# Kernel tuning notes

Measured on AMD Instinct MI355X. Metric: run time of the kernel, lower is better.

## Reference

```python
import jax, jax.numpy as jnp
import numpy as np

N, R, IN_DIM, OUT_DIM, MODE = 8, 256, 64, 64, 32


def setup_inputs() -> dict:
    key = jax.random.key(0)
    k_x, k_w0, k_w1, k_rw, k_rb = jax.random.split(key, 5)
    scale = (1.0 / (IN_DIM * OUT_DIM)) * np.sqrt(IN_DIM + OUT_DIM)
    return {
        "x": jax.random.normal(k_x, (N, R, R, IN_DIM), dtype=jnp.float32),
        # real/imag stacked, matching torch Parameter [m, m, in, out, 2]
        "w0": jax.random.normal(k_w0, (MODE, MODE, IN_DIM, OUT_DIM, 2), dtype=jnp.float32) * scale,
        "w1": jax.random.normal(k_w1, (MODE, MODE, IN_DIM, OUT_DIM, 2), dtype=jnp.float32) * scale,
        # residual Linear: stored as [in, out] (torch keeps [out, in]; math identical)
        "res_w": jax.random.normal(k_rw, (IN_DIM, OUT_DIM), dtype=jnp.float32) * 0.05,
        "res_b": jax.random.normal(k_rb, (OUT_DIM,), dtype=jnp.float32) * 0.05,
    }


def reference(x, w0, w1, res_w, res_b):
    n, r, _, in_dim = x.shape
    m = w0.shape[0]
    rc = r // 2 + 1
    out_dim = w0.shape[3]

    # residual branch (Linear)
    res = jnp.einsum("nhwi,io->nhwo", x, res_w) + res_b  # [N, r, r, out]

    # channels-first for 2D FFT over spatial dims (droprate = 0 -> no dropout)
    xt = jnp.transpose(x, (0, 3, 1, 2))                    # [N, in, r, r]
    x_ft = jnp.fft.rfft2(xt, s=(r, r), norm="ortho")       # [N, in, r, rc] complex

    # gather low-frequency mode blocks: rows [0:m] and [r-m:r], cols [0:m]
    blk0 = x_ft[:, :, :m, :m]                              # [N, in, m, m]
    blk1 = x_ft[:, :, r - m:, :m]                          # [N, in, m, m]

    W0 = w0[..., 0] + 1j * w0[..., 1]                      # [m, m, in, out]
    W1 = w1[..., 0] + 1j * w1[..., 1]

    out0 = jnp.einsum("nixy,xyio->noxy", blk0, W0)         # [N, out, m, m]
    out1 = jnp.einsum("nixy,xyio->noxy", blk1, W1)

    # scatter back into zero-initialized full spectrum
    out_ft = jnp.zeros((n, out_dim, r, rc), dtype=out0.dtype)
    out_ft = out_ft.at[:, :, :m, :m].set(out0)
    out_ft = out_ft.at[:, :, r - m:, :m].set(out1)

    y = jnp.fft.irfft2(out_ft, s=(r, r), norm="ortho")     # [N, out, r, r]
    y = jnp.transpose(y, (0, 2, 3, 1))                     # [N, r, r, out]
    return jax.nn.silu(y + res)
```

## Files before the change

### kernel.cpp

```cpp
#include <hip/hip_runtime.h>
#include <math.h>

#define NN 8
#define RR 256
#define CD 64
#define MM 32
#define KHN 64
#define KWN 32

#define ANG 0.024543692606170259f
#define INVN (1.0f / 65536.0f)

typedef __attribute__((ext_vector_type(4))) float f32x4;
typedef __attribute__((ext_vector_type(8))) short short8;
typedef unsigned short u16;

__device__ inline u16 f2bf(float f) {
    union { float f; unsigned u; } v; v.f = f;
    unsigned r = v.u + 0x7FFF + ((v.u >> 16) & 1);
    return (u16)(r >> 16);
}
__device__ inline unsigned pack2(float a, float b) {
    return (unsigned)f2bf(a) | ((unsigned)f2bf(b) << 16);
}
__device__ inline int swkey(int row) { return (row & 7) ^ ((row >> 3) & 7); }

__global__ __launch_bounds__(256) void k0_tables(u16* __restrict__ A2g,
                                                 u16* __restrict__ A4g,
                                                 u16* __restrict__ T1g,
                                                 u16* __restrict__ T5g,
                                                 const float* __restrict__ res_w,
                                                 u16* __restrict__ RWTg) {
    int gid = blockIdx.x * 256 + threadIdx.x;
    {
        int r = gid >> 9, k = gid & 511;
        int khIdx = r & 63, part = r >> 6;
        int kh = (khIdx < 32) ? khIdx : 192 + khIdx;
        int h = k & 255, kpart = k >> 8;
        float s, c;
        __sincosf((float)((kh * h) & 255) * ANG, &s, &c);
        float v = (part == 0) ? ((kpart == 0) ? c : s)
                              : ((kpart == 0) ? -s : c);
        A2g[gid] = f2bf(v);
    }
    {
        int r = gid >> 7, k = gid & 127;
        int h = r & 255, part = r >> 8;
        int khIdx = k & 63, kpart = k >> 6;
        int kh = (khIdx < 32) ? khIdx : 192 + khIdx;
        float s, c;
        __sincosf((float)((kh * h) & 255) * ANG, &s, &c);
        float v = (part == 0) ? ((kpart == 0) ? c : -s)
                              : ((kpart == 0) ? s : c);
        A4g[gid] = f2bf(v);
    }
    if (gid < 16384) {
        {
            int r = gid >> 8, w = gid & 255;
            float s, c;
            if (r < 32) { __sincosf((float)((r * w) & 255) * ANG, &s, &c); T1g[gid] = f2bf(c); }
            else        { __sincosf((float)(((r - 32) * w) & 255) * ANG, &s, &c); T1g[gid] = f2bf(-s); }
        }
        {
            int w = gid >> 6, c = gid & 63;
            float v;
            if (c == 0) v = 1.0f;
            else if (c < 32) { float s, co; __sincosf((float)((c * w) & 255) * ANG, &s, &co); v = 2.0f * co; }
            else if (c == 32) v = 0.0f;
            else { float s, co; __sincosf((float)(((c - 32) * w) & 255) * ANG, &s, &co); v = -2.0f * s; }
            T5g[gid] = f2bf(v);
        }
    }
    if (gid < 4096) {
        int o = gid >> 6, i = gid & 63;
        RWTg[gid] = f2bf(res_w[i * 64 + o]);
    }
}

__global__ __launch_bounds__(256) void k1_dft_w(const float* __restrict__ x,
                                                const u16* __restrict__ T1g,
                                                u16* __restrict__ X1R,
                                                u16* __restrict__ X1I) {
    __shared__ __align__(16) u16 Bt[64 * 256];
    unsigned* B32 = (unsigned*)Bt;
    int t = threadIdx.x;
    int nh = blockIdx.x;
    const float* xr = x + (size_t)nh * (RR * CD);
#pragma unroll
    for (int it = 0; it < 8; ++it) {
        int idx = t + it * 256;
        int q = idx >> 4;
        int c0 = (idx & 15) * 4;
        float4 f0 = *(const float4*)&xr[(2 * q) * 64 + c0];
        float4 f1 = *(const float4*)&xr[(2 * q + 1) * 64 + c0];
        B32[(c0 + 0) * 128 + (q ^ (swkey(c0 + 0) << 2))] = pack2(f0.x, f1.x);
        B32[(c0 + 1) * 128 + (q ^ (swkey(c0 + 1) << 2))] = pack2(f0.y, f1.y);
        B32[(c0 + 2) * 128 + (q ^ (swkey(c0 + 2) << 2))] = pack2(f0.z, f1.z);
        B32[(c0 + 3) * 128 + (q ^ (swkey(c0 + 3) << 2))] = pack2(f0.w, f1.w);
    }
    __syncthreads();
    int wv = t >> 6, l = t & 63, lm = l & 15, lq = l >> 4;
    f32x4 acc[4];
#pragma unroll
    for (int nt = 0; nt < 4; ++nt) { f32x4 z = {0.f, 0.f, 0.f, 0.f}; acc[nt] = z; }
#pragma unroll
    for (int ks = 0; ks < 8; ++ks) {
        short8 a = *(const short8*)&T1g[(wv * 16 + lm) * 256 + ks * 32 + lq * 8];
#pragma unroll
        for (int nt = 0; nt < 4; ++nt) {
            int c = nt * 16 + lm;
            short8 b = *(const short8*)&Bt[c * 256 + ((ks * 32 + lq * 8) ^ (swkey(c) << 3))];
            acc[nt] = __builtin_amdgcn_mfma_f32_16x16x32_bf16(a, b, acc[nt], 0, 0, 0);
        }
    }
    int n = nh >> 8, h = nh & 255;
#pragma unroll
    for (int nt = 0; nt < 4; ++nt)
#pragma unroll
        for (int r = 0; r < 4; ++r) {
            int kwp = wv * 16 + lq * 4 + r;
            int cc = nt * 16 + lm;
            u16 v = f2bf(acc[nt][r]);
            if (kwp < 32) X1R[(((size_t)n * 32 + kwp) * 256 + h) * 64 + cc] = v;
            else          X1I[(((size_t)n * 32 + (kwp - 32)) * 256 + h) * 64 + cc] = v;
        }
}

__global__ __launch_bounds__(512) void k2_dft_h(const u16* __restrict__ X1R,
                                                const u16* __restrict__ X1I,
                                                const u16* __restrict__ A2g,
                                                float2* __restrict__ X2) {
    __shared__ __align__(16) u16 Bs[2][64 * 128];
    int t = threadIdx.x;
    int n = blockIdx.x >> 5, kw = blockIdx.x & 31;
    const u16* baseR = X1R + ((size_t)n * 32 + kw) * (256 * 64);
    const u16* baseI = X1I + ((size_t)n * 32 + kw) * (256 * 64);
    int wv = t >> 6, l = t & 63, lm = l & 15, lq = l >> 4;
    f32x4 acc[4];
#pragma unroll
    for (int nt = 0; nt < 4; ++nt) { f32x4 z = {0.f, 0.f, 0.f, 0.f}; acc[nt] = z; }

    auto stage = [&](int ck, int buf) {
        const u16* src = ((ck < 2) ? baseR : baseI) + (size_t)(ck & 1) * (128 * 64);
        u16* B = Bs[buf];
#pragma unroll
        for (int it = 0; it < 2; ++it) {
            int idx = t + it * 512;
            int hh = idx >> 3, g = idx & 7;
            short8 v = *(const short8*)&src[hh * 64 + g * 8];
#pragma unroll
            for (int j = 0; j < 8; ++j) {
                int c = g * 8 + j;
                B[c * 128 + (hh ^ (swkey(c) << 3))] = (u16)v[j];
            }
        }
    };
    stage(0, 0);
    __syncthreads();
    for (int ck = 0; ck < 4; ++ck) {
        if (ck < 3) stage(ck + 1, (ck + 1) & 1);
        const u16* B = Bs[ck & 1];
#pragma unroll
        for (int ks = 0; ks < 4; ++ks) {
            short8 a = *(const short8*)&A2g[(wv * 16 + lm) * 512 + ck * 128 + ks * 32 + lq * 8];
#pragma unroll
            for (int nt = 0; nt < 4; ++nt) {
                int c = nt * 16 + lm;
                short8 b = *(const short8*)&B[c * 128 + ((ks * 32 + lq * 8) ^ (swkey(c) << 3))];
                acc[nt] = __builtin_amdgcn_mfma_f32_16x16x32_bf16(a, b, acc[nt], 0, 0, 0);
            }
        }
        __syncthreads();
    }
#pragma unroll
    for (int nt = 0; nt < 4; ++nt)
#pragma unroll
        for (int r = 0; r < 4; ++r) {
            int m = wv * 16 + lq * 4 + r;
            int c = nt * 16 + lm;
            float* dst = (float*)&X2[(((size_t)n * 64 + (m & 63)) * 32 + kw) * 64 + c];
            dst[m >> 6] = acc[nt][r];
        }
}

__global__ __launch_bounds__(256) void k3_spectral(const float2* __restrict__ X2,
                                                   const float* __restrict__ w0,
                                                   const float* __restrict__ w1,
                                                   unsigned* __restrict__ X3b) {
    __shared__ float2 WsP[4096];
    __shared__ float2 XsP[512];
    int t = threadIdx.x;
    int khIdx = blockIdx.x >> 5;
    int kw = blockIdx.x & 31;
    const float* wsrc = (khIdx < 32)
        ? (w0 + (size_t)(khIdx * 32 + kw) * (64 * 64 * 2))
        : (w1 + (size_t)((khIdx - 32) * 32 + kw) * (64 * 64 * 2));
    const float4* wsrc4 = (const float4*)wsrc;
#pragma unroll
    for (int k = 0; k < 8; ++k) {
        int idx = t + k * 256;
        float4 v = wsrc4[idx];
        WsP[2 * idx]     = make_float2(v.x * INVN, v.y * INVN);
        WsP[2 * idx + 1] = make_float2(v.z * INVN, v.w * INVN);
    }
#pragma unroll
    for (int k = 0; k < 2; ++k) {
        int id2 = t + k * 256;
        int n = id2 >> 6, c = id2 & 63;
        XsP[id2] = X2[(((size_t)n * KHN + khIdx) * KWN + kw) * CD + c];
    }
    __syncthreads();
    int o = t & 63;
    int ng = t >> 6;
#pragma unroll
    for (int p = 0; p < 2; ++p) {
        int n = ng + p * 4;
        float aR = 0.f, aI = 0.f;
#pragma unroll 8
        for (int i = 0; i < 64; ++i) {
            float2 xv = XsP[n * 64 + i];
            float2 wv_ = WsP[i * 64 + o];
            aR += xv.x * wv_.x - xv.y * wv_.y;
            aI += xv.x * wv_.y + xv.y * wv_.x;
        }
        X3b[(((size_t)n * 32 + kw) * 64 + khIdx) * 64 + o] = pack2(aR, aI);
    }
}

__global__ __launch_bounds__(256) void k4_idft_h(const unsigned* __restrict__ X3b,
                                                 const u16* __restrict__ A4g,
                                                 u16* __restrict__ Y1R,
                                                 u16* __restrict__ Y1I) {
    __shared__ __align__(16) u16 Bs[64 * 128];
    int t = threadIdx.x;
    int b = blockIdx.x;
    int n = b >> 7, kw = (b >> 2) & 31, mh = (b >> 1) & 1, ac = b & 1;
    const unsigned* src = X3b + ((size_t)n * 32 + kw) * (64 * 64);
#pragma unroll
    for (int it = 0; it < 16; ++it) {
        int khl = (t & 7) + ((it & 7) << 3);
        int o = ((t >> 3) & 31) + ((it >> 3) << 5);
        unsigned v = src[khl * 64 + o];
        int K = swkey(o) << 3;
        Bs[o * 128 + (khl ^ K)]        = (u16)(v & 0xFFFF);
        Bs[o * 128 + ((64 + khl) ^ K)] = (u16)(v >> 16);
    }
    __syncthreads();
    int wv = t >> 6, l = t & 63, lm = l & 15, lq = l >> 4;
    u16* plane = mh ? Y1I : Y1R;
    f32x4 acc[2][4];
#pragma unroll
    for (int mt = 0; mt < 2; ++mt)
#pragma unroll
        for (int nt = 0; nt < 4; ++nt) { f32x4 z = {0.f, 0.f, 0.f, 0.f}; acc[mt][nt] = z; }
#pragma unroll
    for (int ks = 0; ks < 4; ++ks) {
        short8 a0 = *(const short8*)&A4g[(size_t)(mh * 256 + ac * 128 + wv * 32 + lm) * 128 + ks * 32 + lq * 8];
        short8 a1 = *(const short8*)&A4g[(size_t)(mh * 256 + ac * 128 + wv * 32 + 16 + lm) * 128 + ks * 32 + lq * 8];
#pragma unroll
        for (int nt = 0; nt < 4; ++nt) {
            int c = nt * 16 + lm;
            short8 bfr = *(const short8*)&Bs[c * 128 + ((ks * 32 + lq * 8) ^ (swkey(c) << 3))];
            acc[0][nt] = __builtin_amdgcn_mfma_f32_16x16x32_bf16(a0, bfr, acc[0][nt], 0, 0, 0);
            acc[1][nt] = __builtin_amdgcn_mfma_f32_16x16x32_bf16(a1, bfr, acc[1][nt], 0, 0, 0);
        }
    }
#pragma unroll
    for (int mt = 0; mt < 2; ++mt)
#pragma unroll
        for (int nt = 0; nt < 4; ++nt)
#pragma unroll
            for (int r = 0; r < 4; ++r) {
                int h = ac * 128 + wv * 32 + mt * 16 + lq * 4 + r;
                int o = nt * 16 + lm;
                plane[(((size_t)n * 256 + h) * 32 + kw) * 64 + o] = f2bf(acc[mt][nt][r]);
            }
}

__global__ __launch_bounds__(256) void k5_final(const u16* __restrict__ YRp,
                                                const u16* __restrict__ YIp,
                                                const float* __restrict__ x,
                                                const float* __restrict__ res_b,
                                                const u16* __restrict__ T5g,
                                                const u16* __restrict__ RWTg,
                                                float* __restrict__ out) {
    __shared__ __align__(16) u16 Xs[128 * 64];
    __shared__ __align__(16) u16 Bs[64 * 128];
    __shared__ float bs[64];
    unsigned* X32 = (unsigned*)Xs;
    unsigned* B32 = (unsigned*)Bs;
    int t = threadIdx.x;
    int nh = blockIdx.x >> 1, half = blockIdx.x & 1;
    if (t < 64) bs[t] = res_b[t];
    const float* xb = x + ((size_t)nh * 256 + half * 128) * 64;
#pragma unroll
    for (int it = 0; it < 8; ++it) {
        int idx = t + it * 256;
        int wl = idx >> 4, c4 = idx & 15;
        float4 f = *(const float4*)&xb[wl * 64 + c4 * 4];
        uint2 pv; pv.x = pack2(f.x, f.y); pv.y = pack2(f.z, f.w);
        *(uint2*)&X32[wl * 32 + ((2 * c4) ^ (swkey(wl) << 2))] = pv;
    }
    const u16* YR = YRp + (size_t)nh * 2048;
    const u16* YI = YIp + (size_t)nh * 2048;
#pragma unroll
    for (int it = 0; it < 8; ++it) {
        int kw = t >> 3;
        int op = (t & 7) + (it & 3) * 8;
        const u16* P = (it >> 2) ? YI : YR;
        unsigned v = *(const unsigned*)&P[kw * 64 + 2 * op];
        int k = (it >> 2) * 32 + kw;
        int o0 = 2 * op;
        Bs[o0 * 128 + (k ^ (swkey(o0) << 3))]       = (u16)(v & 0xFFFF);
        Bs[(o0 + 1) * 128 + (k ^ (swkey(o0 + 1) << 3))] = (u16)(v >> 16);
    }
#pragma unroll
    for (int it = 0; it < 2; ++it) {
        int idx = t + it * 256;
        int o = idx >> 3, g = idx & 7;
        uint4 v = *(const uint4*)&RWTg[o * 64 + g * 8];
        *(uint4*)&B32[o * 64 + (8 + (g ^ swkey(o))) * 4] = v;
    }
    __syncthreads();
    int wv = t >> 6, l = t & 63, lm = l & 15, lq = l >> 4;
    f32x4 acc[2][4];
#pragma unroll
    for (int mt = 0; mt < 2; ++mt)
#pragma unroll
        for (int nt = 0; nt < 4; ++nt) { f32x4 z = {0.f, 0.f, 0.f, 0.f}; acc[mt][nt] = z; }
#pragma unroll
    for (int ks = 0; ks < 4; ++ks) {
        int r0 = wv * 32 + lm, r1 = r0 + 16;
        short8 a0, a1;
        if (ks < 2) {
            a0 = *(const short8*)&T5g[(half * 128 + r0) * 64 + ks * 32 + lq * 8];
            a1 = *(const short8*)&T5g[(half * 128 + r1) * 64 + ks * 32 + lq * 8];
        } else {
            a0 = *(const short8*)&Xs[r0 * 64 + (((ks - 2) * 32 + lq * 8) ^ (swkey(r0) << 3))];
            a1 = *(const short8*)&Xs[r1 * 64 + (((ks - 2) * 32 + lq * 8) ^ (swkey(r1) << 3))];
        }
#pragma unroll
        for (int nt = 0; nt < 4; ++nt) {
            int c = nt * 16 + lm;
            short8 b = *(const short8*)&Bs[c * 128 + ((ks * 32 + lq * 8) ^ (swkey(c) << 3))];
            acc[0][nt] = __builtin_amdgcn_mfma_f32_16x16x32_bf16(a0, b, acc[0][nt], 0, 0, 0);
            acc[1][nt] = __builtin_amdgcn_mfma_f32_16x16x32_bf16(a1, b, acc[1][nt], 0, 0, 0);
        }
    }
    float* orow = out + ((size_t)nh * 256 + half * 128) * 64;
#pragma unroll
    for (int mt = 0; mt < 2; ++mt)
#pragma unroll
        for (int nt = 0; nt < 4; ++nt)
#pragma unroll
            for (int r = 0; r < 4; ++r) {
                int wloc = wv * 32 + mt * 16 + lq * 4 + r;
                int o = nt * 16 + lm;
                float v = acc[mt][nt][r] + bs[o];
                float sv = v / (1.0f + __expf(-v));
                orow[wloc * 64 + o] = sv;
            }
}

extern "C" void kernel_launch(void* const* d_in, const int* in_sizes, int n_in,
                              void* d_out, int out_size, void* d_ws, size_t ws_size,
                              hipStream_t stream) {
    const float* x     = (const float*)d_in[0];
    const float* w0    = (const float*)d_in[1];
    const float* w1    = (const float*)d_in[2];
    const float* res_w = (const float*)d_in[3];
    const float* res_b = (const float*)d_in[4];
    float* out = (float*)d_out;
    char* ws = (char*)d_ws;
    u16*      X1R  = (u16*)(ws);
    u16*      X1I  = (u16*)(ws + 8388608);
    float2*   X2   = (float2*)(ws + 16777216);
    unsigned* X3b  = (unsigned*)(ws + 25165824);
    u16*      Y1R  = (u16*)(ws + 33554432);
    u16*      Y1I  = (u16*)(ws + 41943040);
    u16*      A2g  = (u16*)(ws + 50331648);
    u16*      A4g  = (u16*)(ws + 50462720);
    u16*      T1g  = (u16*)(ws + 50593792);
    u16*      T5g  = (u16*)(ws + 50626560);
    u16*      RWTg = (u16*)(ws + 50659328);

    k0_tables  <<<256,          256, 0, stream>>>(A2g, A4g, T1g, T5g, res_w, RWTg);
    k1_dft_w   <<<NN * RR,      256, 0, stream>>>(x, T1g, X1R, X1I);
    k2_dft_h   <<<NN * KWN,     512, 0, stream>>>(X1R, X1I, A2g, X2);
    k3_spectral<<<KHN * KWN,    256, 0, stream>>>(X2, w0, w1, X3b);
    k4_idft_h  <<<NN * KWN * 4, 256, 0, stream>>>(X3b, A4g, Y1R, Y1I);
    k5_final   <<<NN * RR * 2,  256, 0, stream>>>(Y1R, Y1I, x, res_b, T5g, RWTg, out);
}
```

Baseline: 352.6 us.

## Fuse six FFT-stage kernels into one cooperative persistent kernel with grid syncs

```diff
diff --git a/kernel.cpp b/kernel.cpp
--- a/kernel.cpp
+++ b/kernel.cpp
@@ -1,5 +1,8 @@
 #include <hip/hip_runtime.h>
+#include <hip/hip_cooperative_groups.h>
 #include <math.h>
+
+namespace cg = cooperative_groups;
 
 #define NN 8
 #define RR 256
@@ -24,6 +27,369 @@
     return (unsigned)f2bf(a) | ((unsigned)f2bf(b) << 16);
 }
 __device__ inline int swkey(int row) { return (row & 7) ^ ((row >> 3) & 7); }
+
+__global__ __launch_bounds__(256, 4) void mega(
+    const float* __restrict__ x, const float* __restrict__ w0,
+    const float* __restrict__ w1, const float* __restrict__ res_w,
+    const float* __restrict__ res_b,
+    u16* __restrict__ X1R, u16* __restrict__ X1I,
+    float2* __restrict__ X2, unsigned* __restrict__ X3b,
+    u16* __restrict__ Y1R, u16* __restrict__ Y1I,
+    u16* __restrict__ A2g, u16* __restrict__ A4g,
+    u16* __restrict__ T1g, u16* __restrict__ T5g,
+    u16* __restrict__ RWTg, float* __restrict__ out)
+{
+    cg::grid_group grid = cg::this_grid();
+    __shared__ __align__(16) unsigned char SMEM[37120];
+    int t = threadIdx.x;
+    int b = blockIdx.x;
+    int G = gridDim.x;
+    int wv = t >> 6, l = t & 63, lm = l & 15, lq = l >> 4;
+
+    {
+        int gid = b * 256 + t;
+        if (gid < 65536) {
+            {
+                int r = gid >> 9, k = gid & 511;
+                int khIdx = r & 63, part = r >> 6;
+                int kh = (khIdx < 32) ? khIdx : 192 + khIdx;
+                int h = k & 255, kpart = k >> 8;
+                float s, c;
+                __sincosf((float)((kh * h) & 255) * ANG, &s, &c);
+                float v = (part == 0) ? ((kpart == 0) ? c : s)
+                                      : ((kpart == 0) ? -s : c);
+                A2g[gid] = f2bf(v);
+            }
+            {
+                int r = gid >> 7, k = gid & 127;
+                int h = r & 255, part = r >> 8;
+                int khIdx = k & 63, kpart = k >> 6;
+                int kh = (khIdx < 32) ? khIdx : 192 + khIdx;
+                float s, c;
+                __sincosf((float)((kh * h) & 255) * ANG, &s, &c);
+                float v = (part == 0) ? ((kpart == 0) ? c : -s)
+                                      : ((kpart == 0) ? s : c);
+                A4g[gid] = f2bf(v);
+            }
+            if (gid < 16384) {
+                {
+                    int r = gid >> 8, w = gid & 255;
+                    float s, c;
+                    if (r < 32) { __sincosf((float)((r * w) & 255) * ANG, &s, &c); T1g[gid] = f2bf(c); }
+                    else        { __sincosf((float)(((r - 32) * w) & 255) * ANG, &s, &c); T1g[gid] = f2bf(-s); }
+                }
+                {
+                    int w = gid >> 6, c = gid & 63;
+                    float v;
+                    if (c == 0) v = 1.0f;
+                    else if (c < 32) { float s, co; __sincosf((float)((c * w) & 255) * ANG, &s, &co); v = 2.0f * co; }
+                    else if (c == 32) v = 0.0f;
+                    else { float s, co; __sincosf((float)(((c - 32) * w) & 255) * ANG, &s, &co); v = -2.0f * s; }
+                    T5g[gid] = f2bf(v);
+                }
+            }
+            if (gid < 4096) {
+                int o = gid >> 6, i = gid & 63;
+                RWTg[gid] = f2bf(res_w[i * 64 + o]);
+            }
+        }
+    }
+    __threadfence();
+    grid.sync();
+
+    {
+        u16* Bt = (u16*)SMEM;
+        unsigned* B32 = (unsigned*)SMEM;
+        for (int nh = b; nh < NN * RR; nh += G) {
+            const float* xr = x + (size_t)nh * (RR * CD);
+#pragma unroll
+            for (int it = 0; it < 8; ++it) {
+                int idx = t + it * 256;
+                int q = idx >> 4;
+                int c0 = (idx & 15) * 4;
+                float4 f0 = *(const float4*)&xr[(2 * q) * 64 + c0];
+                float4 f1 = *(const float4*)&xr[(2 * q + 1) * 64 + c0];
+                B32[(c0 + 0) * 128 + (q ^ (swkey(c0 + 0) << 2))] = pack2(f0.x, f1.x);
+                B32[(c0 + 1) * 128 + (q ^ (swkey(c0 + 1) << 2))] = pack2(f0.y, f1.y);
+                B32[(c0 + 2) * 128 + (q ^ (swkey(c0 + 2) << 2))] = pack2(f0.z, f1.z);
+                B32[(c0 + 3) * 128 + (q ^ (swkey(c0 + 3) << 2))] = pack2(f0.w, f1.w);
+            }
+            __syncthreads();
+            f32x4 acc[4];
+#pragma unroll
+            for (int nt = 0; nt < 4; ++nt) { f32x4 z = {0.f, 0.f, 0.f, 0.f}; acc[nt] = z; }
+#pragma unroll
+            for (int ks = 0; ks < 8; ++ks) {
+                short8 a = *(const short8*)&T1g[(wv * 16 + lm) * 256 + ks * 32 + lq * 8];
+#pragma unroll
+                for (int nt = 0; nt < 4; ++nt) {
+                    int c = nt * 16 + lm;
+                    short8 bf = *(const short8*)&Bt[c * 256 + ((ks * 32 + lq * 8) ^ (swkey(c) << 3))];
+                    acc[nt] = __builtin_amdgcn_mfma_f32_16x16x32_bf16(a, bf, acc[nt], 0, 0, 0);
+                }
+            }
+            int n = nh >> 8, h = nh & 255;
+#pragma unroll
+            for (int nt = 0; nt < 4; ++nt)
+#pragma unroll
+                for (int r = 0; r < 4; ++r) {
+                    int kwp = wv * 16 + lq * 4 + r;
+                    int cc = nt * 16 + lm;
+                    u16 v = f2bf(acc[nt][r]);
+                    if (kwp < 32) X1R[(((size_t)n * 32 + kwp) * 256 + h) * 64 + cc] = v;
+                    else          X1I[(((size_t)n * 32 + (kwp - 32)) * 256 + h) * 64 + cc] = v;
+                }
+            __syncthreads();
+        }
+    }
+    __threadfence();
+    grid.sync();
+
+    {
+        u16* Bs0 = (u16*)SMEM;
+        u16* Bs1 = (u16*)(SMEM + 16384);
+        for (int tile = b; tile < NN * KWN; tile += G) {
+            int n = tile >> 5, kw = tile & 31;
+            const u16* baseR = X1R + ((size_t)n * 32 + kw) * (256 * 64);
+            const u16* baseI = X1I + ((size_t)n * 32 + kw) * (256 * 64);
+            f32x4 acc[2][4];
+#pragma unroll
+            for (int mt = 0; mt < 2; ++mt)
+#pragma unroll
+                for (int nt = 0; nt < 4; ++nt) { f32x4 z = {0.f, 0.f, 0.f, 0.f}; acc[mt][nt] = z; }
+            auto stage = [&](int ck, u16* Bp) {
+                const u16* src = ((ck < 2) ? baseR : baseI) + (size_t)(ck & 1) * (128 * 64);
+                unsigned* B32 = (unsigned*)Bp;
+#pragma unroll
+                for (int it = 0; it < 2; ++it) {
+                    int idx = t + it * 256;
+                    int hh2 = idx >> 3;
+                    int g = idx & 7;
+                    short8 v0 = *(const short8*)&src[(2 * hh2) * 64 + g * 8];
+                    short8 v1 = *(const short8*)&src[(2 * hh2 + 1) * 64 + g * 8];
+#pragma unroll
+                    for (int j = 0; j < 8; ++j) {
+                        int c = g * 8 + j;
+                        B32[c * 64 + (hh2 ^ (swkey(c) << 2))] =
+                            (unsigned)(u16)v0[j] | ((unsigned)(u16)v1[j] << 16);
+                    }
+                }
+            };
+            stage(0, Bs0);
+            __syncthreads();
+            for (int ck = 0; ck < 4; ++ck) {
+                if (ck < 3) stage(ck + 1, ((ck + 1) & 1) ? Bs1 : Bs0);
+                const u16* B = (ck & 1) ? Bs1 : Bs0;
+#pragma unroll
+                for (int ks = 0; ks < 4; ++ks) {
+                    short8 a0 = *(const short8*)&A2g[(wv * 32 + lm) * 512 + ck * 128 + ks * 32 + lq * 8];
+                    short8 a1 = *(const short8*)&A2g[(wv * 32 + 16 + lm) * 512 + ck * 128 + ks * 32 + lq * 8];
+#pragma unroll
+                    for (int nt = 0; nt < 4; ++nt) {
+                        int c = nt * 16 + lm;
+                        short8 bf = *(const short8*)&B[c * 128 + ((ks * 32 + lq * 8) ^ (swkey(c) << 3))];
+                        acc[0][nt] = __builtin_amdgcn_mfma_f32_16x16x32_bf16(a0, bf, acc[0][nt], 0, 0, 0);
+                        acc[1][nt] = __builtin_amdgcn_mfma_f32_16x16x32_bf16(a1, bf, acc[1][nt], 0, 0, 0);
+                    }
+                }
+                __syncthreads();
+            }
+#pragma unroll
+            for (int mt = 0; mt < 2; ++mt)
+#pragma unroll
+                for (int nt = 0; nt < 4; ++nt)
+#pragma unroll
+                    for (int r = 0; r < 4; ++r) {
+                        int m = wv * 32 + mt * 16 + lq * 4 + r;
+                        int c = nt * 16 + lm;
+                        float* dst = (float*)&X2[(((size_t)n * 64 + (m & 63)) * 32 + kw) * 64 + c];
+                        dst[m >> 6] = acc[mt][nt][r];
+                    }
+            __syncthreads();
+        }
+    }
+    __threadfence();
+    grid.sync();
+
+    {
+        float2* WsP = (float2*)SMEM;
+        float2* XsP = (float2*)(SMEM + 32768);
+        for (int tile = b; tile < KHN * KWN; tile += G) {
+            int khIdx = tile >> 5;
+            int kw = tile & 31;
+            const float* wsrc = (khIdx < 32)
+                ? (w0 + (size_t)(khIdx * 32 + kw) * (64 * 64 * 2))
+                : (w1 + (size_t)((khIdx - 32) * 32 + kw) * (64 * 64 * 2));
+            const float4* wsrc4 = (const float4*)wsrc;
+#pragma unroll
+            for (int k = 0; k < 8; ++k) {
+                int idx = t + k * 256;
+                float4 v = wsrc4[idx];
+                WsP[2 * idx]     = make_float2(v.x * INVN, v.y * INVN);
+                WsP[2 * idx + 1] = make_float2(v.z * INVN, v.w * INVN);
+            }
+#pragma unroll
+            for (int k = 0; k < 2; ++k) {
+                int id2 = t + k * 256;
+                int n = id2 >> 6, c = id2 & 63;
+                XsP[id2] = X2[(((size_t)n * KHN + khIdx) * KWN + kw) * CD + c];
+            }
+            __syncthreads();
+            int o = t & 63;
+            int ng = t >> 6;
+#pragma unroll
+            for (int p = 0; p < 2; ++p) {
+                int n = ng + p * 4;
+                float aR = 0.f, aI = 0.f;
+#pragma unroll 8
+                for (int i = 0; i < 64; ++i) {
+                    float2 xv = XsP[n * 64 + i];
+                    float2 wv_ = WsP[i * 64 + o];
+                    aR += xv.x * wv_.x - xv.y * wv_.y;
+                    aI += xv.x * wv_.y + xv.y * wv_.x;
+                }
+                X3b[(((size_t)n * 32 + kw) * 64 + khIdx) * 64 + o] = pack2(aR, aI);
+            }
+            __syncthreads();
+        }
+    }
+    __threadfence();
+    grid.sync();
+
+    {
+        u16* Bs = (u16*)SMEM;
+        unsigned* B32 = (unsigned*)SMEM;
+        for (int tile = b; tile < NN * KWN * 4; tile += G) {
+            int n = tile >> 7, kw = (tile >> 2) & 31, mh = (tile >> 1) & 1, ac = tile & 1;
+            const unsigned* src = X3b + ((size_t)n * 32 + kw) * (64 * 64);
+#pragma unroll
+            for (int it = 0; it < 8; ++it) {
+                int idx = t + it * 256;
+                int khl2 = idx >> 6;
+                int o = idx & 63;
+                unsigned vA = src[(2 * khl2) * 64 + o];
+                unsigned vB = src[(2 * khl2 + 1) * 64 + o];
+                int K = swkey(o) << 2;
+                B32[o * 64 + (khl2 ^ K)]        = (vA & 0xFFFF) | (vB << 16);
+                B32[o * 64 + ((32 + khl2) ^ K)] = (vA >> 16) | (vB & 0xFFFF0000u);
+            }
+            __syncthreads();
+            u16* plane = mh ? Y1I : Y1R;
+            f32x4 acc[2][4];
+#pragma unroll
+            for (int mt = 0; mt < 2; ++mt)
+#pragma unroll
+                for (int nt = 0; nt < 4; ++nt) { f32x4 z = {0.f, 0.f, 0.f, 0.f}; acc[mt][nt] = z; }
+#pragma unroll
+            for (int ks = 0; ks < 4; ++ks) {
+                short8 a0 = *(const short8*)&A4g[(size_t)(mh * 256 + ac * 128 + wv * 32 + lm) * 128 + ks * 32 + lq * 8];
+                short8 a1 = *(const short8*)&A4g[(size_t)(mh * 256 + ac * 128 + wv * 32 + 16 + lm) * 128 + ks * 32 + lq * 8];
+#pragma unroll
+                for (int nt = 0; nt < 4; ++nt) {
+                    int c = nt * 16 + lm;
+                    short8 bfr = *(const short8*)&Bs[c * 128 + ((ks * 32 + lq * 8) ^ (swkey(c) << 3))];
+                    acc[0][nt] = __builtin_amdgcn_mfma_f32_16x16x32_bf16(a0, bfr, acc[0][nt], 0, 0, 0);
+                    acc[1][nt] = __builtin_amdgcn_mfma_f32_16x16x32_bf16(a1, bfr, acc[1][nt], 0, 0, 0);
+                }
+            }
+#pragma unroll
+            for (int mt = 0; mt < 2; ++mt)
+#pragma unroll
+                for (int nt = 0; nt < 4; ++nt)
+#pragma unroll
+                    for (int r = 0; r < 4; ++r) {
+                        int h = ac * 128 + wv * 32 + mt * 16 + lq * 4 + r;
+                        int o = nt * 16 + lm;
+                        plane[(((size_t)n * 256 + h) * 32 + kw) * 64 + o] = f2bf(acc[mt][nt][r]);
+                    }
+            __syncthreads();
+        }
+    }
+    __threadfence();
+    grid.sync();
+
+    {
+        u16* Xs = (u16*)SMEM;
+        u16* Bs = (u16*)(SMEM + 16384);
+        float* bsm = (float*)(SMEM + 32768);
+        unsigned* X32 = (unsigned*)Xs;
+        unsigned* B32 = (unsigned*)Bs;
+        if (t < 64) bsm[t] = res_b[t];
+        for (int bb = b; bb < NN * RR * 2; bb += G) {
+            int nh = bb >> 1, half = bb & 1;
+            const float* xb = x + ((size_t)nh * 256 + half * 128) * 64;
+#pragma unroll
+            for (int it = 0; it < 8; ++it) {
+                int idx = t + it * 256;
+                int wl = idx >> 4, c4 = idx & 15;
+                float4 f = *(const float4*)&xb[wl * 64 + c4 * 4];
+                uint2 pv; pv.x = pack2(f.x, f.y); pv.y = pack2(f.z, f.w);
+                *(uint2*)&X32[wl * 32 + ((2 * c4) ^ (swkey(wl) << 2))] = pv;
+            }
+            const u16* YR = Y1R + (size_t)nh * 2048;
+            const u16* YI = Y1I + (size_t)nh * 2048;
+#pragma unroll
+            for (int it = 0; it < 4; ++it) {
+                int part = it >> 1;
+                int kw2 = t >> 4;
+                int opb = (t & 15) + (it & 1) * 16;
+                const u16* P = part ? YI : YR;
+                unsigned vA = *(const unsigned*)&P[(2 * kw2) * 64 + 2 * opb];
+                unsigned vB = *(const unsigned*)&P[(2 * kw2 + 1) * 64 + 2 * opb];
+                int o0 = 2 * opb;
+                int k2 = part * 16 + kw2;
+                B32[o0 * 64 + (k2 ^ (swkey(o0) << 2))]       = (vA & 0xFFFF) | (vB << 16);
+                B32[(o0 + 1) * 64 + (k2 ^ (swkey(o0 + 1) << 2))] = (vA >> 16) | (vB & 0xFFFF0000u);
+            }
+#pragma unroll
+            for (int it = 0; it < 2; ++it) {
+                int idx = t + it * 256;
+                int o = idx >> 3, g = idx & 7;
+                uint4 v = *(const uint4*)&RWTg[o * 64 + g * 8];
+                *(uint4*)&B32[o * 64 + (8 + (g ^ swkey(o))) * 4] = v;
+            }
+            __syncthreads();
+            f32x4 acc[2][4];
+#pragma unroll
+            for (int mt = 0; mt < 2; ++mt)
+#pragma unroll
+                for (int nt = 0; nt < 4; ++nt) { f32x4 z = {0.f, 0.f, 0.f, 0.f}; acc[mt][nt] = z; }
+#pragma unroll
+            for (int ks = 0; ks < 4; ++ks) {
+                int r0 = wv * 32 + lm, r1 = r0 + 16;
+                short8 a0, a1;
+                if (ks < 2) {
+                    a0 = *(const short8*)&T5g[(half * 128 + r0) * 64 + ks * 32 + lq * 8];
+                    a1 = *(const short8*)&T5g[(half * 128 + r1) * 64 + ks * 32 + lq * 8];
+                } else {
+                    a0 = *(const short8*)&Xs[r0 * 64 + (((ks - 2) * 32 + lq * 8) ^ (swkey(r0) << 3))];
+                    a1 = *(const short8*)&Xs[r1 * 64 + (((ks - 2) * 32 + lq * 8) ^ (swkey(r1) << 3))];
+                }
+#pragma unroll
+                for (int nt = 0; nt < 4; ++nt) {
+                    int c = nt * 16 + lm;
+                    short8 bf = *(const short8*)&Bs[c * 128 + ((ks * 32 + lq * 8) ^ (swkey(c) << 3))];
+                    acc[0][nt] = __builtin_amdgcn_mfma_f32_16x16x32_bf16(a0, bf, acc[0][nt], 0, 0, 0);
+                    acc[1][nt] = __builtin_amdgcn_mfma_f32_16x16x32_bf16(a1, bf, acc[1][nt], 0, 0, 0);
+                }
+            }
+            float* orow = out + ((size_t)nh * 256 + half * 128) * 64;
+#pragma unroll
+            for (int mt = 0; mt < 2; ++mt)
+#pragma unroll
+                for (int nt = 0; nt < 4; ++nt)
+#pragma unroll
+                    for (int r = 0; r < 4; ++r) {
+                        int wloc = wv * 32 + mt * 16 + lq * 4 + r;
+                        int o = nt * 16 + lm;
+                        float v = acc[mt][nt][r] + bsm[o];
+                        float sv = v / (1.0f + __expf(-v));
+                        orow[wloc * 64 + o] = sv;
+                    }
+            __syncthreads();
+        }
+    }
+}
 
 __global__ __launch_bounds__(256) void k0_tables(u16* __restrict__ A2g,
                                                  u16* __restrict__ A4g,
@@ -39,8 +405,7 @@
         int h = k & 255, kpart = k >> 8;
         float s, c;
         __sincosf((float)((kh * h) & 255) * ANG, &s, &c);
-        float v = (part == 0) ? ((kpart == 0) ? c : s)
-                              : ((kpart == 0) ? -s : c);
+        float v = (part == 0) ? ((kpart == 0) ? c : s) : ((kpart == 0) ? -s : c);
         A2g[gid] = f2bf(v);
     }
     {
@@ -50,8 +415,7 @@
         int kh = (khIdx < 32) ? khIdx : 192 + khIdx;
         float s, c;
         __sincosf((float)((kh * h) & 255) * ANG, &s, &c);
-        float v = (part == 0) ? ((kpart == 0) ? c : -s)
-                              : ((kpart == 0) ? s : c);
+        float v = (part == 0) ? ((kpart == 0) ? c : -s) : ((kpart == 0) ? s : c);
         A4g[gid] = f2bf(v);
     }
     if (gid < 16384) {
@@ -109,8 +473,8 @@
 #pragma unroll
         for (int nt = 0; nt < 4; ++nt) {
             int c = nt * 16 + lm;
-            short8 b = *(const short8*)&Bt[c * 256 + ((ks * 32 + lq * 8) ^ (swkey(c) << 3))];
-            acc[nt] = __builtin_amdgcn_mfma_f32_16x16x32_bf16(a, b, acc[nt], 0, 0, 0);
+            short8 bf = *(const short8*)&Bt[c * 256 + ((ks * 32 + lq * 8) ^ (swkey(c) << 3))];
+            acc[nt] = __builtin_amdgcn_mfma_f32_16x16x32_bf16(a, bf, acc[nt], 0, 0, 0);
         }
     }
     int n = nh >> 8, h = nh & 255;
@@ -139,7 +503,6 @@
     f32x4 acc[4];
 #pragma unroll
     for (int nt = 0; nt < 4; ++nt) { f32x4 z = {0.f, 0.f, 0.f, 0.f}; acc[nt] = z; }
-
     auto stage = [&](int ck, int buf) {
         const u16* src = ((ck < 2) ? baseR : baseI) + (size_t)(ck & 1) * (128 * 64);
         u16* B = Bs[buf];
@@ -166,8 +529,8 @@
 #pragma unroll
             for (int nt = 0; nt < 4; ++nt) {
                 int c = nt * 16 + lm;
-                short8 b = *(const short8*)&B[c * 128 + ((ks * 32 + lq * 8) ^ (swkey(c) << 3))];
-                acc[nt] = __builtin_amdgcn_mfma_f32_16x16x32_bf16(a, b, acc[nt], 0, 0, 0);
+                short8 bf = *(const short8*)&B[c * 128 + ((ks * 32 + lq * 8) ^ (swkey(c) << 3))];
+                acc[nt] = __builtin_amdgcn_mfma_f32_16x16x32_bf16(a, bf, acc[nt], 0, 0, 0);
             }
         }
         __syncthreads();
@@ -232,18 +595,21 @@
                                                  u16* __restrict__ Y1R,
                                                  u16* __restrict__ Y1I) {
     __shared__ __align__(16) u16 Bs[64 * 128];
+    unsigned* B32 = (unsigned*)Bs;
     int t = threadIdx.x;
     int b = blockIdx.x;
     int n = b >> 7, kw = (b >> 2) & 31, mh = (b >> 1) & 1, ac = b & 1;
     const unsigned* src = X3b + ((size_t)n * 32 + kw) * (64 * 64);
 #pragma unroll
-    for (int it = 0; it < 16; ++it) {
-        int khl = (t & 7) + ((it & 7) << 3);
-        int o = ((t >> 3) & 31) + ((it >> 3) << 5);
-        unsigned v = src[khl * 64 + o];
-        int K = swkey(o) << 3;
-        Bs[o * 128 + (khl ^ K)]        = (u16)(v & 0xFFFF);
-        Bs[o * 128 + ((64 + khl) ^ K)] = (u16)(v >> 16);
+    for (int it = 0; it < 8; ++it) {
+        int idx = t + it * 256;
+        int khl2 = idx >> 6;
+        int o = idx & 63;
+        unsigned vA = src[(2 * khl2) * 64 + o];
+        unsigned vB = src[(2 * khl2 + 1) * 64 + o];
+        int K = swkey(o) << 2;
+        B32[o * 64 + (khl2 ^ K)]        = (vA & 0xFFFF) | (vB << 16);
+        B32[o * 64 + ((32 + khl2) ^ K)] = (vA >> 16) | (vB & 0xFFFF0000u);
     }
     __syncthreads();
     int wv = t >> 6, l = t & 63, lm = l & 15, lq = l >> 4;
@@ -304,15 +670,17 @@
     const u16* YR = YRp + (size_t)nh * 2048;
     const u16* YI = YIp + (size_t)nh * 2048;
 #pragma unroll
-    for (int it = 0; it < 8; ++it) {
-        int kw = t >> 3;
-        int op = (t & 7) + (it & 3) * 8;
-        const u16* P = (it >> 2) ? YI : YR;
-        unsigned v = *(const unsigned*)&P[kw * 64 + 2 * op];
-        int k = (it >> 2) * 32 + kw;
-        int o0 = 2 * op;
-        Bs[o0 * 128 + (k ^ (swkey(o0) << 3))]       = (u16)(v & 0xFFFF);
-        Bs[(o0 + 1) * 128 + (k ^ (swkey(o0 + 1) << 3))] = (u16)(v >> 16);
+    for (int it = 0; it < 4; ++it) {
+        int part = it >> 1;
+        int kw2 = t >> 4;
+        int opb = (t & 15) + (it & 1) * 16;
+        const u16* P = part ? YI : YR;
+        unsigned vA = *(const unsigned*)&P[(2 * kw2) * 64 + 2 * opb];
+        unsigned vB = *(const unsigned*)&P[(2 * kw2 + 1) * 64 + 2 * opb];
+        int o0 = 2 * opb;
+        int k2 = part * 16 + kw2;
+        B32[o0 * 64 + (k2 ^ (swkey(o0) << 2))]       = (vA & 0xFFFF) | (vB << 16);
+        B32[(o0 + 1) * 64 + (k2 ^ (swkey(o0 + 1) << 2))] = (vA >> 16) | (vB & 0xFFFF0000u);
     }
 #pragma unroll
     for (int it = 0; it < 2; ++it) {
@@ -342,9 +710,9 @@
 #pragma unroll
         for (int nt = 0; nt < 4; ++nt) {
             int c = nt * 16 + lm;
-            short8 b = *(const short8*)&Bs[c * 128 + ((ks * 32 + lq * 8) ^ (swkey(c) << 3))];
-            acc[0][nt] = __builtin_amdgcn_mfma_f32_16x16x32_bf16(a0, b, acc[0][nt], 0, 0, 0);
-            acc[1][nt] = __builtin_amdgcn_mfma_f32_16x16x32_bf16(a1, b, acc[1][nt], 0, 0, 0);
+            short8 bf = *(const short8*)&Bs[c * 128 + ((ks * 32 + lq * 8) ^ (swkey(c) << 3))];
+            acc[0][nt] = __builtin_amdgcn_mfma_f32_16x16x32_bf16(a0, bf, acc[0][nt], 0, 0, 0);
+            acc[1][nt] = __builtin_amdgcn_mfma_f32_16x16x32_bf16(a1, bf, acc[1][nt], 0, 0, 0);
         }
     }
     float* orow = out + ((size_t)nh * 256 + half * 128) * 64;
@@ -384,10 +752,27 @@
     u16*      T5g  = (u16*)(ws + 50626560);
     u16*      RWTg = (u16*)(ws + 50659328);
 
-    k0_tables  <<<256,          256, 0, stream>>>(A2g, A4g, T1g, T5g, res_w, RWTg);
-    k1_dft_w   <<<NN * RR,      256, 0, stream>>>(x, T1g, X1R, X1I);
-    k2_dft_h   <<<NN * KWN,     512, 0, stream>>>(X1R, X1I, A2g, X2);
-    k3_spectral<<<KHN * KWN,    256, 0, stream>>>(X2, w0, w1, X3b);
-    k4_idft_h  <<<NN * KWN * 4, 256, 0, stream>>>(X3b, A4g, Y1R, Y1I);
-    k5_final   <<<NN * RR * 2,  256, 0, stream>>>(Y1R, Y1I, x, res_b, T5g, RWTg, out);
-}
+    static int G = 0;
+    if (G == 0) {
+        int nb = 0;
+        if (hipOccupancyMaxActiveBlocksPerMultiprocessor(&nb, mega, 256, 0) != hipSuccess || nb < 1)
+            nb = 1;
+        if (nb > 4) nb = 4;
+        G = nb * 256;
+    }
+
+    void* args[] = { (void*)&x, (void*)&w0, (void*)&w1, (void*)&res_w, (void*)&res_b,
+                     (void*)&X1R, (void*)&X1I, (void*)&X2, (void*)&X3b,
+                     (void*)&Y1R, (void*)&Y1I, (void*)&A2g, (void*)&A4g,
+                     (void*)&T1g, (void*)&T5g, (void*)&RWTg, (void*)&out };
+    hipError_t e = hipLaunchCooperativeKernel((const void*)mega, dim3(G), dim3(256),
+                                              args, 0, stream);
+    if (e != hipSuccess) {
+        k0_tables  <<<256,          256, 0, stream>>>(A2g, A4g, T1g, T5g, res_w, RWTg);
+        k1_dft_w   <<<NN * RR,      256, 0, stream>>>(x, T1g, X1R, X1I);
+        k2_dft_h   <<<NN * KWN,     512, 0, stream>>>(X1R, X1I, A2g, X2);
+        k3_spectral<<<KHN * KWN,    256, 0, stream>>>(X2, w0, w1, X3b);
+        k4_idft_h  <<<NN * KWN * 4, 256, 0, stream>>>(X3b, A4g, Y1R, Y1I);
+        k5_final   <<<NN * RR * 2,  256, 0, stream>>>(Y1R, Y1I, x, res_b, T5g, RWTg, out);
+    }
+}
```

Result: slower. 895.4 us (+153.9%).

## Fuse forward H-DFT, spectral mixing and inverse H-DFT into one kernel

Applied to the files above, without the earlier changes.

```diff
diff --git a/kernel.cpp b/kernel.cpp
--- a/kernel.cpp
+++ b/kernel.cpp
@@ -39,8 +39,7 @@
         int h = k & 255, kpart = k >> 8;
         float s, c;
         __sincosf((float)((kh * h) & 255) * ANG, &s, &c);
-        float v = (part == 0) ? ((kpart == 0) ? c : s)
-                              : ((kpart == 0) ? -s : c);
+        float v = (part == 0) ? ((kpart == 0) ? c : s) : ((kpart == 0) ? -s : c);
         A2g[gid] = f2bf(v);
     }
     {
@@ -50,8 +49,7 @@
         int kh = (khIdx < 32) ? khIdx : 192 + khIdx;
         float s, c;
         __sincosf((float)((kh * h) & 255) * ANG, &s, &c);
-        float v = (part == 0) ? ((kpart == 0) ? c : -s)
-                              : ((kpart == 0) ? s : c);
+        float v = (part == 0) ? ((kpart == 0) ? c : -s) : ((kpart == 0) ? s : c);
         A4g[gid] = f2bf(v);
     }
     if (gid < 16384) {
@@ -109,8 +107,8 @@
 #pragma unroll
         for (int nt = 0; nt < 4; ++nt) {
             int c = nt * 16 + lm;
-            short8 b = *(const short8*)&Bt[c * 256 + ((ks * 32 + lq * 8) ^ (swkey(c) << 3))];
-            acc[nt] = __builtin_amdgcn_mfma_f32_16x16x32_bf16(a, b, acc[nt], 0, 0, 0);
+            short8 bf = *(const short8*)&Bt[c * 256 + ((ks * 32 + lq * 8) ^ (swkey(c) << 3))];
+            acc[nt] = __builtin_amdgcn_mfma_f32_16x16x32_bf16(a, bf, acc[nt], 0, 0, 0);
         }
     }
     int n = nh >> 8, h = nh & 255;
@@ -126,23 +124,30 @@
         }
 }
 
-__global__ __launch_bounds__(512) void k2_dft_h(const u16* __restrict__ X1R,
-                                                const u16* __restrict__ X1I,
-                                                const u16* __restrict__ A2g,
-                                                float2* __restrict__ X2) {
-    __shared__ __align__(16) u16 Bs[2][64 * 128];
+__global__ __launch_bounds__(512) void k234(const u16* __restrict__ X1R,
+                                            const u16* __restrict__ X1I,
+                                            const u16* __restrict__ A2g,
+                                            const float* __restrict__ w0,
+                                            const float* __restrict__ w1,
+                                            const u16* __restrict__ A4g,
+                                            u16* __restrict__ Y1R,
+                                            u16* __restrict__ Y1I) {
+    __shared__ __align__(16) unsigned char SMEM[49664];
+    u16* Bs0 = (u16*)SMEM;
+    u16* Bs1 = (u16*)(SMEM + 16384);
+    float* Xsp = (float*)SMEM;
+    u16* X3s = (u16*)(SMEM + 33280);
     int t = threadIdx.x;
     int n = blockIdx.x >> 5, kw = blockIdx.x & 31;
     const u16* baseR = X1R + ((size_t)n * 32 + kw) * (256 * 64);
     const u16* baseI = X1I + ((size_t)n * 32 + kw) * (256 * 64);
     int wv = t >> 6, l = t & 63, lm = l & 15, lq = l >> 4;
+
     f32x4 acc[4];
 #pragma unroll
     for (int nt = 0; nt < 4; ++nt) { f32x4 z = {0.f, 0.f, 0.f, 0.f}; acc[nt] = z; }
-
-    auto stage = [&](int ck, int buf) {
+    auto stage = [&](int ck, u16* B) {
         const u16* src = ((ck < 2) ? baseR : baseI) + (size_t)(ck & 1) * (128 * 64);
-        u16* B = Bs[buf];
 #pragma unroll
         for (int it = 0; it < 2; ++it) {
             int idx = t + it * 512;
@@ -155,19 +160,19 @@
             }
         }
     };
-    stage(0, 0);
+    stage(0, Bs0);
     __syncthreads();
     for (int ck = 0; ck < 4; ++ck) {
-        if (ck < 3) stage(ck + 1, (ck + 1) & 1);
-        const u16* B = Bs[ck & 1];
+        if (ck < 3) stage(ck + 1, ((ck + 1) & 1) ? Bs1 : Bs0);
+        const u16* B = (ck & 1) ? Bs1 : Bs0;
 #pragma unroll
         for (int ks = 0; ks < 4; ++ks) {
             short8 a = *(const short8*)&A2g[(wv * 16 + lm) * 512 + ck * 128 + ks * 32 + lq * 8];
 #pragma unroll
             for (int nt = 0; nt < 4; ++nt) {
                 int c = nt * 16 + lm;
-                short8 b = *(const short8*)&B[c * 128 + ((ks * 32 + lq * 8) ^ (swkey(c) << 3))];
-                acc[nt] = __builtin_amdgcn_mfma_f32_16x16x32_bf16(a, b, acc[nt], 0, 0, 0);
+                short8 bf = *(const short8*)&B[c * 128 + ((ks * 32 + lq * 8) ^ (swkey(c) << 3))];
+                acc[nt] = __builtin_amdgcn_mfma_f32_16x16x32_bf16(a, bf, acc[nt], 0, 0, 0);
             }
         }
         __syncthreads();
@@ -178,103 +183,62 @@
         for (int r = 0; r < 4; ++r) {
             int m = wv * 16 + lq * 4 + r;
             int c = nt * 16 + lm;
-            float* dst = (float*)&X2[(((size_t)n * 64 + (m & 63)) * 32 + kw) * 64 + c];
-            dst[m >> 6] = acc[nt][r];
-        }
-}
-
-__global__ __launch_bounds__(256) void k3_spectral(const float2* __restrict__ X2,
-                                                   const float* __restrict__ w0,
-                                                   const float* __restrict__ w1,
-                                                   unsigned* __restrict__ X3b) {
-    __shared__ float2 WsP[4096];
-    __shared__ float2 XsP[512];
-    int t = threadIdx.x;
-    int khIdx = blockIdx.x >> 5;
-    int kw = blockIdx.x & 31;
-    const float* wsrc = (khIdx < 32)
-        ? (w0 + (size_t)(khIdx * 32 + kw) * (64 * 64 * 2))
-        : (w1 + (size_t)((khIdx - 32) * 32 + kw) * (64 * 64 * 2));
-    const float4* wsrc4 = (const float4*)wsrc;
-#pragma unroll
-    for (int k = 0; k < 8; ++k) {
-        int idx = t + k * 256;
-        float4 v = wsrc4[idx];
-        WsP[2 * idx]     = make_float2(v.x * INVN, v.y * INVN);
-        WsP[2 * idx + 1] = make_float2(v.z * INVN, v.w * INVN);
-    }
-#pragma unroll
-    for (int k = 0; k < 2; ++k) {
-        int id2 = t + k * 256;
-        int n = id2 >> 6, c = id2 & 63;
-        XsP[id2] = X2[(((size_t)n * KHN + khIdx) * KWN + kw) * CD + c];
-    }
-    __syncthreads();
-    int o = t & 63;
-    int ng = t >> 6;
-#pragma unroll
-    for (int p = 0; p < 2; ++p) {
-        int n = ng + p * 4;
-        float aR = 0.f, aI = 0.f;
+            Xsp[(m >> 6) * 4160 + (m & 63) * 65 + c] = acc[nt][r];
+        }
+    __syncthreads();
+
+    {
+        int o = t & 63, g = t >> 6;
+#pragma unroll
+        for (int jj = 0; jj < 8; ++jj) {
+            int kh = g * 8 + jj;
+            const float2* wb = (const float2*)((kh < 32)
+                ? (w0 + (size_t)(kh * 32 + kw) * (64 * 64 * 2))
+                : (w1 + (size_t)((kh - 32) * 32 + kw) * (64 * 64 * 2)));
+            float aR = 0.f, aI = 0.f;
 #pragma unroll 8
-        for (int i = 0; i < 64; ++i) {
-            float2 xv = XsP[n * 64 + i];
-            float2 wv_ = WsP[i * 64 + o];
-            aR += xv.x * wv_.x - xv.y * wv_.y;
-            aI += xv.x * wv_.y + xv.y * wv_.x;
-        }
-        X3b[(((size_t)n * 32 + kw) * 64 + khIdx) * 64 + o] = pack2(aR, aI);
-    }
-}
-
-__global__ __launch_bounds__(256) void k4_idft_h(const unsigned* __restrict__ X3b,
-                                                 const u16* __restrict__ A4g,
-                                                 u16* __restrict__ Y1R,
-                                                 u16* __restrict__ Y1I) {
-    __shared__ __align__(16) u16 Bs[64 * 128];
-    int t = threadIdx.x;
-    int b = blockIdx.x;
-    int n = b >> 7, kw = (b >> 2) & 31, mh = (b >> 1) & 1, ac = b & 1;
-    const unsigned* src = X3b + ((size_t)n * 32 + kw) * (64 * 64);
-#pragma unroll
-    for (int it = 0; it < 16; ++it) {
-        int khl = (t & 7) + ((it & 7) << 3);
-        int o = ((t >> 3) & 31) + ((it >> 3) << 5);
-        unsigned v = src[khl * 64 + o];
-        int K = swkey(o) << 3;
-        Bs[o * 128 + (khl ^ K)]        = (u16)(v & 0xFFFF);
-        Bs[o * 128 + ((64 + khl) ^ K)] = (u16)(v >> 16);
-    }
-    __syncthreads();
-    int wv = t >> 6, l = t & 63, lm = l & 15, lq = l >> 4;
-    u16* plane = mh ? Y1I : Y1R;
-    f32x4 acc[2][4];
-#pragma unroll
-    for (int mt = 0; mt < 2; ++mt)
-#pragma unroll
-        for (int nt = 0; nt < 4; ++nt) { f32x4 z = {0.f, 0.f, 0.f, 0.f}; acc[mt][nt] = z; }
-#pragma unroll
-    for (int ks = 0; ks < 4; ++ks) {
-        short8 a0 = *(const short8*)&A4g[(size_t)(mh * 256 + ac * 128 + wv * 32 + lm) * 128 + ks * 32 + lq * 8];
-        short8 a1 = *(const short8*)&A4g[(size_t)(mh * 256 + ac * 128 + wv * 32 + 16 + lm) * 128 + ks * 32 + lq * 8];
-#pragma unroll
-        for (int nt = 0; nt < 4; ++nt) {
-            int c = nt * 16 + lm;
-            short8 bfr = *(const short8*)&Bs[c * 128 + ((ks * 32 + lq * 8) ^ (swkey(c) << 3))];
-            acc[0][nt] = __builtin_amdgcn_mfma_f32_16x16x32_bf16(a0, bfr, acc[0][nt], 0, 0, 0);
-            acc[1][nt] = __builtin_amdgcn_mfma_f32_16x16x32_bf16(a1, bfr, acc[1][nt], 0, 0, 0);
-        }
-    }
-#pragma unroll
-    for (int mt = 0; mt < 2; ++mt)
-#pragma unroll
-        for (int nt = 0; nt < 4; ++nt)
-#pragma unroll
-            for (int r = 0; r < 4; ++r) {
-                int h = ac * 128 + wv * 32 + mt * 16 + lq * 4 + r;
-                int o = nt * 16 + lm;
-                plane[(((size_t)n * 256 + h) * 32 + kw) * 64 + o] = f2bf(acc[mt][nt][r]);
-            }
+            for (int i = 0; i < 64; ++i) {
+                float xr = Xsp[kh * 65 + i];
+                float xi = Xsp[4160 + kh * 65 + i];
+                float2 w2 = wb[i * 64 + o];
+                aR += xr * w2.x - xi * w2.y;
+                aI += xr * w2.y + xi * w2.x;
+            }
+            int s3 = swkey(o) << 3;
+            X3s[o * 128 + (kh ^ s3)]        = f2bf(aR * INVN);
+            X3s[o * 128 + ((64 + kh) ^ s3)] = f2bf(aI * INVN);
+        }
+    }
+    __syncthreads();
+
+#pragma unroll
+    for (int mh = 0; mh < 2; ++mh) {
+        u16* plane = mh ? Y1I : Y1R;
+#pragma unroll
+        for (int ac = 0; ac < 2; ++ac) {
+            f32x4 acc2[4];
+#pragma unroll
+            for (int nt = 0; nt < 4; ++nt) { f32x4 z = {0.f, 0.f, 0.f, 0.f}; acc2[nt] = z; }
+#pragma unroll
+            for (int ks = 0; ks < 4; ++ks) {
+                short8 a = *(const short8*)&A4g[(size_t)(mh * 256 + ac * 128 + wv * 16 + lm) * 128 + ks * 32 + lq * 8];
+#pragma unroll
+                for (int nt = 0; nt < 4; ++nt) {
+                    int c = nt * 16 + lm;
+                    short8 bfr = *(const short8*)&X3s[c * 128 + ((ks * 32 + lq * 8) ^ (swkey(c) << 3))];
+                    acc2[nt] = __builtin_amdgcn_mfma_f32_16x16x32_bf16(a, bfr, acc2[nt], 0, 0, 0);
+                }
+            }
+#pragma unroll
+            for (int nt = 0; nt < 4; ++nt)
+#pragma unroll
+                for (int r = 0; r < 4; ++r) {
+                    int h = ac * 128 + wv * 16 + lq * 4 + r;
+                    int o = nt * 16 + lm;
+                    plane[(((size_t)n * 256 + h) * 32 + kw) * 64 + o] = f2bf(acc2[nt][r]);
+                }
+        }
+    }
 }
 
 __global__ __launch_bounds__(256) void k5_final(const u16* __restrict__ YRp,
@@ -304,15 +268,17 @@
     const u16* YR = YRp + (size_t)nh * 2048;
     const u16* YI = YIp + (size_t)nh * 2048;
 #pragma unroll
-    for (int it = 0; it < 8; ++it) {
-        int kw = t >> 3;
-        int op = (t & 7) + (it & 3) * 8;
-        const u16* P = (it >> 2) ? YI : YR;
-        unsigned v = *(const unsigned*)&P[kw * 64 + 2 * op];
-        int k = (it >> 2) * 32 + kw;
-        int o0 = 2 * op;
-        Bs[o0 * 128 + (k ^ (swkey(o0) << 3))]       = (u16)(v & 0xFFFF);
-        Bs[(o0 + 1) * 128 + (k ^ (swkey(o0 + 1) << 3))] = (u16)(v >> 16);
+    for (int it = 0; it < 4; ++it) {
+        int part = it >> 1;
+        int kw2 = t >> 4;
+        int opb = (t & 15) + (it & 1) * 16;
+        const u16* P = part ? YI : YR;
+        unsigned vA = *(const unsigned*)&P[(2 * kw2) * 64 + 2 * opb];
+        unsigned vB = *(const unsigned*)&P[(2 * kw2 + 1) * 64 + 2 * opb];
+        int o0 = 2 * opb;
+        int k2 = part * 16 + kw2;
+        B32[o0 * 64 + (k2 ^ (swkey(o0) << 2))]           = (vA & 0xFFFF) | (vB << 16);
+        B32[(o0 + 1) * 64 + (k2 ^ (swkey(o0 + 1) << 2))] = (vA >> 16) | (vB & 0xFFFF0000u);
     }
 #pragma unroll
     for (int it = 0; it < 2; ++it) {
@@ -342,9 +308,9 @@
 #pragma unroll
         for (int nt = 0; nt < 4; ++nt) {
             int c = nt * 16 + lm;
-            short8 b = *(const short8*)&Bs[c * 128 + ((ks * 32 + lq * 8) ^ (swkey(c) << 3))];
-            acc[0][nt] = __builtin_amdgcn_mfma_f32_16x16x32_bf16(a0, b, acc[0][nt], 0, 0, 0);
-            acc[1][nt] = __builtin_amdgcn_mfma_f32_16x16x32_bf16(a1, b, acc[1][nt], 0, 0, 0);
+            short8 bf = *(const short8*)&Bs[c * 128 + ((ks * 32 + lq * 8) ^ (swkey(c) << 3))];
+            acc[0][nt] = __builtin_amdgcn_mfma_f32_16x16x32_bf16(a0, bf, acc[0][nt], 0, 0, 0);
+            acc[1][nt] = __builtin_amdgcn_mfma_f32_16x16x32_bf16(a1, bf, acc[1][nt], 0, 0, 0);
         }
     }
     float* orow = out + ((size_t)nh * 256 + half * 128) * 64;
@@ -372,22 +338,18 @@
     const float* res_b = (const float*)d_in[4];
     float* out = (float*)d_out;
     char* ws = (char*)d_ws;
-    u16*      X1R  = (u16*)(ws);
-    u16*      X1I  = (u16*)(ws + 8388608);
-    float2*   X2   = (float2*)(ws + 16777216);
-    unsigned* X3b  = (unsigned*)(ws + 25165824);
-    u16*      Y1R  = (u16*)(ws + 33554432);
-    u16*      Y1I  = (u16*)(ws + 41943040);
-    u16*      A2g  = (u16*)(ws + 50331648);
-    u16*      A4g  = (u16*)(ws + 50462720);
-    u16*      T1g  = (u16*)(ws + 50593792);
-    u16*      T5g  = (u16*)(ws + 50626560);
-    u16*      RWTg = (u16*)(ws + 50659328);
-
-    k0_tables  <<<256,          256, 0, stream>>>(A2g, A4g, T1g, T5g, res_w, RWTg);
-    k1_dft_w   <<<NN * RR,      256, 0, stream>>>(x, T1g, X1R, X1I);
-    k2_dft_h   <<<NN * KWN,     512, 0, stream>>>(X1R, X1I, A2g, X2);
-    k3_spectral<<<KHN * KWN,    256, 0, stream>>>(X2, w0, w1, X3b);
-    k4_idft_h  <<<NN * KWN * 4, 256, 0, stream>>>(X3b, A4g, Y1R, Y1I);
-    k5_final   <<<NN * RR * 2,  256, 0, stream>>>(Y1R, Y1I, x, res_b, T5g, RWTg, out);
-}
+    u16* X1R  = (u16*)(ws);
+    u16* X1I  = (u16*)(ws + 8388608);
+    u16* Y1R  = (u16*)(ws + 33554432);
+    u16* Y1I  = (u16*)(ws + 41943040);
+    u16* A2g  = (u16*)(ws + 50331648);
+    u16* A4g  = (u16*)(ws + 50462720);
+    u16* T1g  = (u16*)(ws + 50593792);
+    u16* T5g  = (u16*)(ws + 50626560);
+    u16* RWTg = (u16*)(ws + 50659328);
+
+    k0_tables<<<256,         256, 0, stream>>>(A2g, A4g, T1g, T5g, res_w, RWTg);
+    k1_dft_w <<<NN * RR,     256, 0, stream>>>(x, T1g, X1R, X1I);
+    k234     <<<NN * KWN,    512, 0, stream>>>(X1R, X1I, A2g, w0, w1, A4g, Y1R, Y1I);
+    k5_final <<<NN * RR * 2, 256, 0, stream>>>(Y1R, Y1I, x, res_b, T5g, RWTg, out);
+}
```

Measured after the change: 378.5 us. 7.4% more time.
